# Performance work log

Hardware: AMD Instinct MI355X
Metric: run time of the kernel (lower is better)

## Reference

```python
import jax, jax.numpy as jnp
import numpy as np

BETA = 0.95
THR = 1.0  # snntorch Leaky default threshold

# Heaviside spike with ATan surrogate gradient (snntorch default, alpha=2):
# d/dx = 1 / (1 + (pi*x)^2)
@jax.custom_vjp
def spike_fn(x):
    return (x > 0).astype(x.dtype)

def _spike_fwd(x):
    return spike_fn(x), x

def _spike_bwd(x, g):
    return (g / (1.0 + (jnp.pi * x) ** 2),)

spike_fn.defvjp(_spike_fwd, _spike_bwd)


def setup_inputs() -> dict:
    key = jax.random.key(0)
    ks = jax.random.split(key, 5)
    T, B, D_in, D_h, D_out = 25, 4096, 784, 1000, 10
    x = jax.random.normal(ks[0], (T, B, D_in), dtype=jnp.float32)
    # Kaiming-uniform-ish init like nn.Linear
    w1 = jax.random.uniform(ks[1], (D_h, D_in), jnp.float32, -1, 1) / np.sqrt(D_in)
    b1 = jax.random.uniform(ks[2], (D_h,), jnp.float32, -1, 1) / np.sqrt(D_in)
    w2 = jax.random.uniform(ks[3], (D_out, D_h), jnp.float32, -1, 1) / np.sqrt(D_h)
    b2 = jax.random.uniform(ks[4], (D_out,), jnp.float32, -1, 1) / np.sqrt(D_h)
    return {"x": x, "w1": w1, "b1": b1, "w2": w2, "b2": b2}


def reference(x, w1, b1, w2, b2):
    B = x.shape[1]
    mem1_0 = jnp.zeros((B, w1.shape[0]), x.dtype)
    mem2_0 = jnp.zeros((B, w2.shape[0]), x.dtype)

    def step(carry, xt):
        mem1, mem2 = carry
        # layer 1: Linear + Leaky (reset-by-subtraction, reset from prior mem)
        cur1 = xt @ w1.T + b1
        reset1 = spike_fn(mem1 - THR)
        mem1 = BETA * mem1 + cur1 - reset1 * THR
        spk1 = spike_fn(mem1 - THR)
        # layer 2
        cur2 = spk1 @ w2.T + b2
        reset2 = spike_fn(mem2 - THR)
        mem2 = BETA * mem2 + cur2 - reset2 * THR
        spk2 = spike_fn(mem2 - THR)
        return (mem1, mem2), spk2

    (mem1, mem2), spk_rec = jax.lax.scan(step, (mem1_0, mem2_0), x)
    return spk_rec, mem2
```

## Files before the change

### kernel.cpp

```cpp
#include <hip/hip_runtime.h>

typedef _Float16 f16;
typedef _Float16 f16x4 __attribute__((ext_vector_type(4)));
typedef _Float16 f16x8 __attribute__((ext_vector_type(8)));
typedef float f32x4 __attribute__((ext_vector_type(4)));

#define T_STEPS 25
#define BATCH   4096
#define DIN     784
#define DH      1000
#define HP      1024
#define DOUT    10
#define MROWS   (T_STEPS * BATCH)
#define KSEG    800
#define KA      (2 * KSEG)
#define KB      (3 * KSEG)
#define NTILES  (KB / 32)

__global__ void aconv_kernel(const float* __restrict__ x, f16* __restrict__ Ah)
{
    const int total = MROWS * 200;
    for (int idx = blockIdx.x * blockDim.x + threadIdx.x; idx < total;
         idx += gridDim.x * blockDim.x) {
        const int r  = idx / 200;
        const int c4 = (idx - r * 200) * 4;
        f16x4 hi, lo;
        if (c4 < DIN) {
            const float4 v = *(const float4*)(x + (size_t)r * DIN + c4);
            const float vv[4] = {v.x, v.y, v.z, v.w};
            #pragma unroll
            for (int j = 0; j < 4; ++j) {
                f16 h = (f16)vv[j];
                hi[j] = h;
                lo[j] = (f16)(vv[j] - (float)h);
            }
        } else {
            #pragma unroll
            for (int j = 0; j < 4; ++j) { hi[j] = (f16)0.f; lo[j] = (f16)0.f; }
        }
        *(f16x4*)(Ah + (size_t)r * KA + c4)        = hi;
        *(f16x4*)(Ah + (size_t)r * KA + KSEG + c4) = lo;
    }
}

__global__ void wconv_kernel(const float* __restrict__ w1, const float* __restrict__ b1,
                             const float* __restrict__ w2,
                             f16* __restrict__ Wh, float* __restrict__ b1p,
                             float* __restrict__ w2t)
{
    const int stride = gridDim.x * blockDim.x;
    const int tid0 = blockIdx.x * blockDim.x + threadIdx.x;
    for (int idx = tid0; idx < HP * KB; idx += stride) {
        const int n  = idx / KB;
        const int k  = idx - n * KB;
        const int seg = k / KSEG;
        const int kc  = k - seg * KSEG;
        float w = (n < DH && kc < DIN) ? w1[n * DIN + kc] : 0.f;
        f16 h = (f16)w;
        Wh[idx] = (seg < 2) ? h : (f16)(w - (float)h);
    }
    for (int idx = tid0; idx < HP; idx += stride)
        b1p[idx] = (idx < DH) ? b1[idx] : 0.f;
    for (int idx = tid0; idx < HP * DOUT; idx += stride) {
        const int h = idx / DOUT;
        const int o = idx - h * DOUT;
        w2t[idx] = (h < DH) ? w2[o * DH + h] : 0.f;
    }
}

#define GL(gp, ldsoff) __builtin_amdgcn_global_load_lds( \
    (const __attribute__((address_space(1))) void*)(gp), \
    (__attribute__((address_space(3))) void*)(lds + (ldsoff)), 16, 0, 0)

#define STAGE_A(tt) do { \
    const int ak_ = (((tt) < 50) ? (tt) : ((tt) - 50)) * 32; \
    GL(Ag + ak_,            ((tt) & 3) * 8192 + widoff); \
    GL(Ag + ak_ + 128 * KA, ((tt) & 3) * 8192 + 4096 + widoff); } while (0)
#define STAGE_B(tt) do { \
    const int bk_ = (tt) * 32; \
    GL(Bg + bk_,                     32768 + ((tt) & 3) * 8192 + widoff); \
    GL(Bg + bk_ + (size_t)128 * KB,  32768 + ((tt) & 3) * 8192 + 4096 + widoff); } while (0)

#define MFMA16(A0, A1, A2, A3, B0, B1, B2, B3, M0) \
    acc[M0+0][0] = __builtin_amdgcn_mfma_f32_16x16x32_f16(A0, B0, acc[M0+0][0], 0, 0, 0); \
    acc[M0+0][1] = __builtin_amdgcn_mfma_f32_16x16x32_f16(A0, B1, acc[M0+0][1], 0, 0, 0); \
    acc[M0+0][2] = __builtin_amdgcn_mfma_f32_16x16x32_f16(A0, B2, acc[M0+0][2], 0, 0, 0); \
    acc[M0+0][3] = __builtin_amdgcn_mfma_f32_16x16x32_f16(A0, B3, acc[M0+0][3], 0, 0, 0); \
    acc[M0+1][0] = __builtin_amdgcn_mfma_f32_16x16x32_f16(A1, B0, acc[M0+1][0], 0, 0, 0); \
    acc[M0+1][1] = __builtin_amdgcn_mfma_f32_16x16x32_f16(A1, B1, acc[M0+1][1], 0, 0, 0); \
    acc[M0+1][2] = __builtin_amdgcn_mfma_f32_16x16x32_f16(A1, B2, acc[M0+1][2], 0, 0, 0); \
    acc[M0+1][3] = __builtin_amdgcn_mfma_f32_16x16x32_f16(A1, B3, acc[M0+1][3], 0, 0, 0); \
    acc[M0+2][0] = __builtin_amdgcn_mfma_f32_16x16x32_f16(A2, B0, acc[M0+2][0], 0, 0, 0); \
    acc[M0+2][1] = __builtin_amdgcn_mfma_f32_16x16x32_f16(A2, B1, acc[M0+2][1], 0, 0, 0); \
    acc[M0+2][2] = __builtin_amdgcn_mfma_f32_16x16x32_f16(A2, B2, acc[M0+2][2], 0, 0, 0); \
    acc[M0+2][3] = __builtin_amdgcn_mfma_f32_16x16x32_f16(A2, B3, acc[M0+2][3], 0, 0, 0); \
    acc[M0+3][0] = __builtin_amdgcn_mfma_f32_16x16x32_f16(A3, B0, acc[M0+3][0], 0, 0, 0); \
    acc[M0+3][1] = __builtin_amdgcn_mfma_f32_16x16x32_f16(A3, B1, acc[M0+3][1], 0, 0, 0); \
    acc[M0+3][2] = __builtin_amdgcn_mfma_f32_16x16x32_f16(A3, B2, acc[M0+3][2], 0, 0, 0); \
    acc[M0+3][3] = __builtin_amdgcn_mfma_f32_16x16x32_f16(A3, B3, acc[M0+3][3], 0, 0, 0);

#define BODY(tt, aI0,aI1,aI2,aI3, bI0,bI1,bI2,bI3, aO0,aO1,aO2,aO3, bO0,bO1,bO2,bO3, STG, VMWSTR) do { \
    const int bcur = ((tt) & 3) * 8192; \
    const int bnxt = (((tt) + 1) & 3) * 8192; \
    if (STG) { STAGE_A((tt) + 3); STAGE_B((tt) + 3); } \
    asm volatile("s_waitcnt lgkmcnt(0)" ::: "memory");    \
    __builtin_amdgcn_sched_barrier(0); \
    ah0 = *(const f16x8*)(lds + bcur + aoffb + 4 * 512); \
    ah1 = *(const f16x8*)(lds + bcur + aoffb + 5 * 512); \
    ah2 = *(const f16x8*)(lds + bcur + aoffb + 6 * 512); \
    ah3 = *(const f16x8*)(lds + bcur + aoffb + 7 * 512); \
    __builtin_amdgcn_sched_barrier(0); \
    __builtin_amdgcn_s_setprio(1); \
    MFMA16(aI0, aI1, aI2, aI3, bI0, bI1, bI2, bI3, 0)     \
    __builtin_amdgcn_s_setprio(0); \
    asm volatile("s_waitcnt lgkmcnt(0)" ::: "memory");    \
    __builtin_amdgcn_sched_barrier(0); \
    asm volatile(VMWSTR ::: "memory"); \
    __builtin_amdgcn_s_barrier();                         \
    aO0 = *(const f16x8*)(lds + bnxt + aoffb + 0 * 512); \
    aO1 = *(const f16x8*)(lds + bnxt + aoffb + 1 * 512); \
    aO2 = *(const f16x8*)(lds + bnxt + aoffb + 2 * 512); \
    aO3 = *(const f16x8*)(lds + bnxt + aoffb + 3 * 512); \
    bO0 = *(const f16x8*)(lds + 32768 + bnxt + boffb + 0 * 512); \
    bO1 = *(const f16x8*)(lds + 32768 + bnxt + boffb + 1 * 512); \
    bO2 = *(const f16x8*)(lds + 32768 + bnxt + boffb + 2 * 512); \
    bO3 = *(const f16x8*)(lds + 32768 + bnxt + boffb + 3 * 512); \
    __builtin_amdgcn_sched_barrier(0); \
    __builtin_amdgcn_s_setprio(1); \
    MFMA16(ah0, ah1, ah2, ah3, bI0, bI1, bI2, bI3, 4)     \
    __builtin_amdgcn_s_setprio(0); \
} while (0)

#define BODY_(...) BODY(__VA_ARGS__)

#define SET_A aA0,aA1,aA2,aA3, bA0,bA1,bA2,bA3
#define SET_B aB0,aB1,aB2,aB3, bB0,bB1,bB2,bB3

__global__ __launch_bounds__(512, 2)
void gemm_kernel(const f16* __restrict__ A, const f16* __restrict__ B,
                 const float* __restrict__ bias, float* __restrict__ C)
{
    __shared__ f16 lds[65536];

    const int bid = blockIdx.x;
    const int swz = (bid & 7) * 200 + (bid >> 3);
    const int mt = swz >> 2;
    const int nt = swz & 3;
    const size_t rowBase = (size_t)mt * 256;
    const int colBase = nt * 256;

    const int tid  = threadIdx.x;
    const int wid  = tid >> 6;
    const int lane = tid & 63;
    const int wm = wid >> 2;
    const int wn = wid & 3;

    const int srow = tid >> 2;
    const int g = (tid & 3) ^ ((tid >> 3) & 3);
    const f16* Ag = A + (rowBase + srow) * KA + g * 8;
    const f16* Bg = B + (size_t)(colBase + srow) * KB + g * 8;
    const int widoff = wid * 512;

    const int cq = (lane >> 4) ^ (((lane & 15) >> 1) & 3);
    const int aoffb = (wm * 128 + (lane & 15)) * 32 + cq * 8;
    const int boffb = (wn * 64  + (lane & 15)) * 32 + cq * 8;

    f32x4 acc[8][4];
    #pragma unroll
    for (int m = 0; m < 8; ++m)
        #pragma unroll
        for (int n = 0; n < 4; ++n)
            acc[m][n] = (f32x4){0.f, 0.f, 0.f, 0.f};

    f16x8 aA0, aA1, aA2, aA3, bA0, bA1, bA2, bA3;
    f16x8 aB0, aB1, aB2, aB3, bB0, bB1, bB2, bB3;
    f16x8 ah0, ah1, ah2, ah3;

    STAGE_A(0); STAGE_B(0);
    STAGE_A(1); STAGE_B(1);
    STAGE_A(2); STAGE_B(2);
    asm volatile("s_waitcnt vmcnt(8)" ::: "memory");
    __builtin_amdgcn_s_barrier();
    aA0 = *(const f16x8*)(lds + aoffb + 0 * 512);
    aA1 = *(const f16x8*)(lds + aoffb + 1 * 512);
    aA2 = *(const f16x8*)(lds + aoffb + 2 * 512);
    aA3 = *(const f16x8*)(lds + aoffb + 3 * 512);
    bA0 = *(const f16x8*)(lds + 32768 + boffb + 0 * 512);
    bA1 = *(const f16x8*)(lds + 32768 + boffb + 1 * 512);
    bA2 = *(const f16x8*)(lds + 32768 + boffb + 2 * 512);
    bA3 = *(const f16x8*)(lds + 32768 + boffb + 3 * 512);

    for (int t = 0; t < NTILES - 3; t += 2) {
        BODY_(t,     SET_A, SET_B, 1, "s_waitcnt vmcnt(8)");
        BODY_(t + 1, SET_B, SET_A, 1, "s_waitcnt vmcnt(8)");
    }
    BODY_(NTILES - 3, SET_A, SET_B, 0, "s_waitcnt vmcnt(4)");
    BODY_(NTILES - 2, SET_B, SET_A, 0, "s_waitcnt vmcnt(0)");
    {
        const int bcur = ((NTILES - 1) & 3) * 8192;
        asm volatile("s_waitcnt lgkmcnt(0)" ::: "memory");
        __builtin_amdgcn_sched_barrier(0);
        ah0 = *(const f16x8*)(lds + bcur + aoffb + 4 * 512);
        ah1 = *(const f16x8*)(lds + bcur + aoffb + 5 * 512);
        ah2 = *(const f16x8*)(lds + bcur + aoffb + 6 * 512);
        ah3 = *(const f16x8*)(lds + bcur + aoffb + 7 * 512);
        __builtin_amdgcn_sched_barrier(0);
        MFMA16(aA0, aA1, aA2, aA3, bA0, bA1, bA2, bA3, 0)
        asm volatile("s_waitcnt lgkmcnt(0)" ::: "memory");
        __builtin_amdgcn_sched_barrier(0);
        MFMA16(ah0, ah1, ah2, ah3, bA0, bA1, bA2, bA3, 4)
    }

    const int c_col0 = colBase + wn * 64 + (lane & 15);
    const size_t c_row0 = rowBase + wm * 128 + (lane >> 4) * 4;
    #pragma unroll
    for (int n = 0; n < 4; ++n) {
        const int gcol = c_col0 + n * 16;
        const float bv = bias[gcol];
        #pragma unroll
        for (int m = 0; m < 8; ++m) {
            const size_t grow = c_row0 + m * 16;
            #pragma unroll
            for (int r = 0; r < 4; ++r)
                C[(grow + r) * HP + gcol] = acc[m][n][r] + bv;
        }
    }
}

__global__ __launch_bounds__(256)
void phase2_kernel(const float* __restrict__ cur1, const float* __restrict__ w2t,
                   const float* __restrict__ b2, float* __restrict__ out)
{
    __shared__ float w2s[HP * DOUT];
    const int tid = threadIdx.x;
    for (int i = tid; i < HP * DOUT; i += 256) w2s[i] = w2t[i];

    const int lane = tid & 63;
    const int wave = tid >> 6;
    const int b = blockIdx.x * 4 + wave;

    float m1[16];
    #pragma unroll
    for (int i = 0; i < 16; ++i) m1[i] = 0.f;
    float m2[DOUT], b2r[DOUT];
    #pragma unroll
    for (int o = 0; o < DOUT; ++o) { m2[o] = 0.f; b2r[o] = b2[o]; }
    __syncthreads();

    for (int t = 0; t < T_STEPS; ++t) {
        const float* cr = cur1 + ((size_t)t * BATCH + b) * HP;
        float p[DOUT];
        #pragma unroll
        for (int o = 0; o < DOUT; ++o) p[o] = 0.f;

        #pragma unroll
        for (int c = 0; c < 4; ++c) {
            const float4 cu = *(const float4*)(cr + c * 256 + lane * 4);
            const float cv[4] = {cu.x, cu.y, cu.z, cu.w};
            #pragma unroll
            for (int j = 0; j < 4; ++j) {
                const float mo = m1[c * 4 + j];
                const float rs = (mo > 1.0f) ? 1.0f : 0.0f;
                const float mn = 0.95f * mo + cv[j] - rs;
                m1[c * 4 + j] = mn;
                if (mn > 1.0f) {
                    const float* wr = w2s + (c * 256 + lane * 4 + j) * DOUT;
                    #pragma unroll
                    for (int o = 0; o < DOUT; ++o) p[o] += wr[o];
                }
            }
        }
        #pragma unroll
        for (int o = 0; o < DOUT; ++o) {
            float v = p[o];
            #pragma unroll
            for (int msk = 32; msk > 0; msk >>= 1) v += __shfl_xor(v, msk, 64);
            p[o] = v;
        }
        #pragma unroll
        for (int o = 0; o < DOUT; ++o) {
            const float cur2 = p[o] + b2r[o];
            const float mo = m2[o];
            const float rs = (mo > 1.0f) ? 1.0f : 0.0f;
            m2[o] = 0.95f * mo + cur2 - rs;
        }
        if (lane < DOUT)
            out[(size_t)t * (BATCH * DOUT) + (size_t)b * DOUT + lane] =
                (m2[lane] > 1.0f) ? 1.0f : 0.0f;
    }
    if (lane < DOUT)
        out[(size_t)T_STEPS * BATCH * DOUT + (size_t)b * DOUT + lane] = m2[lane];
}

extern "C" void kernel_launch(void* const* d_in, const int* in_sizes, int n_in,
                              void* d_out, int out_size, void* d_ws, size_t ws_size,
                              hipStream_t stream)
{
    const float* x  = (const float*)d_in[0];
    const float* w1 = (const float*)d_in[1];
    const float* b1 = (const float*)d_in[2];
    const float* w2 = (const float*)d_in[3];
    const float* b2 = (const float*)d_in[4];
    float* out = (float*)d_out;

    char* wsb = (char*)d_ws;
    f16*   Ah   = (f16*)(wsb);
    f16*   Wh   = (f16*)(wsb + 327680000);
    float* cur1 = (float*)(wsb + 327680000 + 4915200);
    float* b1p  = (float*)(wsb + 327680000 + 4915200 + 419430400);
    float* w2t  = (float*)(wsb + 327680000 + 4915200 + 419430400 + 4096);

    aconv_kernel<<<4096, 256, 0, stream>>>(x, Ah);
    wconv_kernel<<<1024, 256, 0, stream>>>(w1, b1, w2, Wh, b1p, w2t);
    gemm_kernel<<<1600, 512, 0, stream>>>(Ah, Wh, b1p, cur1);
    phase2_kernel<<<1024, 256, 0, stream>>>(cur1, w2t, b2, out);
}
```

Baseline: 772.0 us.

## Switch GEMM to 64-wide K tiles with double-buffered LDS staging

The main GEMM now stages 64-wide K tiles into two LDS buffers instead of 32-wide tiles in a four-deep ring, with an 8-wide XOR swizzle for the new row pitch. The weight matrix is padded to 2432 columns so the K loop divides evenly into 38 tiles, and the workspace offsets are adjusted to match. The aim is to halve the number of barrier and wait points per unit of K and to give each wave more MFMA work between synchronisations. In exchange, prefetch runs only one tile ahead, with a full vmcnt(0) wait each iteration, so global-load latency may be less well hidden.

```diff
diff --git a/kernel.cpp b/kernel.cpp
--- a/kernel.cpp
+++ b/kernel.cpp
@@ -15,7 +15,8 @@
 #define KSEG    800
 #define KA      (2 * KSEG)
 #define KB      (3 * KSEG)
-#define NTILES  (KB / 32)
+#define WROW    2432
+#define NT64    38
 
 __global__ void aconv_kernel(const float* __restrict__ x, f16* __restrict__ Ah)
 {
@@ -50,14 +51,18 @@
 {
     const int stride = gridDim.x * blockDim.x;
     const int tid0 = blockIdx.x * blockDim.x + threadIdx.x;
-    for (int idx = tid0; idx < HP * KB; idx += stride) {
-        const int n  = idx / KB;
-        const int k  = idx - n * KB;
-        const int seg = k / KSEG;
-        const int kc  = k - seg * KSEG;
-        float w = (n < DH && kc < DIN) ? w1[n * DIN + kc] : 0.f;
-        f16 h = (f16)w;
-        Wh[idx] = (seg < 2) ? h : (f16)(w - (float)h);
+    for (int idx = tid0; idx < HP * WROW; idx += stride) {
+        const int n  = idx / WROW;
+        const int k  = idx - n * WROW;
+        f16 v = (f16)0.f;
+        if (k < KB) {
+            const int seg = k / KSEG;
+            const int kc  = k - seg * KSEG;
+            float w = (n < DH && kc < DIN) ? w1[n * DIN + kc] : 0.f;
+            f16 h = (f16)w;
+            v = (seg < 2) ? h : (f16)(w - (float)h);
+        }
+        Wh[idx] = v;
     }
     for (int idx = tid0; idx < HP; idx += stride)
         b1p[idx] = (idx < DH) ? b1[idx] : 0.f;
@@ -72,14 +77,18 @@
     (const __attribute__((address_space(1))) void*)(gp), \
     (__attribute__((address_space(3))) void*)(lds + (ldsoff)), 16, 0, 0)
 
-#define STAGE_A(tt) do { \
-    const int ak_ = (((tt) < 50) ? (tt) : ((tt) - 50)) * 32; \
-    GL(Ag + ak_,            ((tt) & 3) * 8192 + widoff); \
-    GL(Ag + ak_ + 128 * KA, ((tt) & 3) * 8192 + 4096 + widoff); } while (0)
-#define STAGE_B(tt) do { \
-    const int bk_ = (tt) * 32; \
-    GL(Bg + bk_,                     32768 + ((tt) & 3) * 8192 + widoff); \
-    GL(Bg + bk_ + (size_t)128 * KB,  32768 + ((tt) & 3) * 8192 + 4096 + widoff); } while (0)
+#define STAGE64(tt) do { \
+    const int _buf = ((tt) & 1) * 16384; \
+    const int _ak  = (((tt) < 25) ? (tt) : ((tt) - 25)) * 64; \
+    const int _bk  = (tt) * 64; \
+    GL(Ag + _ak + 0 * 64 * KA,   _buf + 0 * 4096 + widoff); \
+    GL(Ag + _ak + 1 * 64 * KA,   _buf + 1 * 4096 + widoff); \
+    GL(Ag + _ak + 2 * 64 * KA,   _buf + 2 * 4096 + widoff); \
+    GL(Ag + _ak + 3 * 64 * KA,   _buf + 3 * 4096 + widoff); \
+    GL(Bg + _bk + 0 * 64 * WROW, 32768 + _buf + 0 * 4096 + widoff); \
+    GL(Bg + _bk + 1 * 64 * WROW, 32768 + _buf + 1 * 4096 + widoff); \
+    GL(Bg + _bk + 2 * 64 * WROW, 32768 + _buf + 2 * 4096 + widoff); \
+    GL(Bg + _bk + 3 * 64 * WROW, 32768 + _buf + 3 * 4096 + widoff); } while (0)
 
 #define MFMA16(A0, A1, A2, A3, B0, B1, B2, B3, M0) \
     acc[M0+0][0] = __builtin_amdgcn_mfma_f32_16x16x32_f16(A0, B0, acc[M0+0][0], 0, 0, 0); \
@@ -99,42 +108,65 @@
     acc[M0+3][2] = __builtin_amdgcn_mfma_f32_16x16x32_f16(A3, B2, acc[M0+3][2], 0, 0, 0); \
     acc[M0+3][3] = __builtin_amdgcn_mfma_f32_16x16x32_f16(A3, B3, acc[M0+3][3], 0, 0, 0);
 
-#define BODY(tt, aI0,aI1,aI2,aI3, bI0,bI1,bI2,bI3, aO0,aO1,aO2,aO3, bO0,bO1,bO2,bO3, STG, VMWSTR) do { \
-    const int bcur = ((tt) & 3) * 8192; \
-    const int bnxt = (((tt) + 1) & 3) * 8192; \
-    if (STG) { STAGE_A((tt) + 3); STAGE_B((tt) + 3); } \
-    asm volatile("s_waitcnt lgkmcnt(0)" ::: "memory");    \
-    __builtin_amdgcn_sched_barrier(0); \
-    ah0 = *(const f16x8*)(lds + bcur + aoffb + 4 * 512); \
-    ah1 = *(const f16x8*)(lds + bcur + aoffb + 5 * 512); \
-    ah2 = *(const f16x8*)(lds + bcur + aoffb + 6 * 512); \
-    ah3 = *(const f16x8*)(lds + bcur + aoffb + 7 * 512); \
+#define RD(off) (*(const f16x8*)(lds + (off)))
+
+#define BODY64(tt, STG) do { \
+    const int bufc = ((tt) & 1) * 16384; \
+    f16x8 b00, b01, b02, b03, a00, a01, a02, a03, a10, a11, a12, a13; \
+    f16x8 b10, b11, b12, b13, c00, c01, c02, c03, c10, c11, c12, c13; \
+    if (STG) STAGE64((tt) + 1); \
+     \
+    b00 = RD(bbase + bufc + 0 * 1024 + cA0); \
+    b01 = RD(bbase + bufc + 1 * 1024 + cA0); \
+    b02 = RD(bbase + bufc + 2 * 1024 + cA0); \
+    b03 = RD(bbase + bufc + 3 * 1024 + cA0); \
+    a00 = RD(abase + bufc + 0 * 1024 + cA0); \
+    a01 = RD(abase + bufc + 1 * 1024 + cA0); \
+    a02 = RD(abase + bufc + 2 * 1024 + cA0); \
+    a03 = RD(abase + bufc + 3 * 1024 + cA0); \
+    a10 = RD(abase + bufc + 4096 + 0 * 1024 + cA0); \
+    a11 = RD(abase + bufc + 4096 + 1 * 1024 + cA0); \
+    a12 = RD(abase + bufc + 4096 + 2 * 1024 + cA0); \
+    a13 = RD(abase + bufc + 4096 + 3 * 1024 + cA0); \
+    asm volatile("s_waitcnt lgkmcnt(4)" ::: "memory");   \
     __builtin_amdgcn_sched_barrier(0); \
     __builtin_amdgcn_s_setprio(1); \
-    MFMA16(aI0, aI1, aI2, aI3, bI0, bI1, bI2, bI3, 0)     \
+    MFMA16(a00, a01, a02, a03, b00, b01, b02, b03, 0) \
     __builtin_amdgcn_s_setprio(0); \
-    asm volatile("s_waitcnt lgkmcnt(0)" ::: "memory");    \
-    __builtin_amdgcn_sched_barrier(0); \
-    asm volatile(VMWSTR ::: "memory"); \
-    __builtin_amdgcn_s_barrier();                         \
-    aO0 = *(const f16x8*)(lds + bnxt + aoffb + 0 * 512); \
-    aO1 = *(const f16x8*)(lds + bnxt + aoffb + 1 * 512); \
-    aO2 = *(const f16x8*)(lds + bnxt + aoffb + 2 * 512); \
-    aO3 = *(const f16x8*)(lds + bnxt + aoffb + 3 * 512); \
-    bO0 = *(const f16x8*)(lds + 32768 + bnxt + boffb + 0 * 512); \
-    bO1 = *(const f16x8*)(lds + 32768 + bnxt + boffb + 1 * 512); \
-    bO2 = *(const f16x8*)(lds + 32768 + bnxt + boffb + 2 * 512); \
-    bO3 = *(const f16x8*)(lds + 32768 + bnxt + boffb + 3 * 512); \
+    asm volatile("s_waitcnt lgkmcnt(0)" ::: "memory");   \
+    __builtin_amdgcn_sched_barrier(0); \
+     \
+    b10 = RD(bbase + bufc + 0 * 1024 + cA1); \
+    b11 = RD(bbase + bufc + 1 * 1024 + cA1); \
+    b12 = RD(bbase + bufc + 2 * 1024 + cA1); \
+    b13 = RD(bbase + bufc + 3 * 1024 + cA1); \
+    c00 = RD(abase + bufc + 0 * 1024 + cA1); \
+    c01 = RD(abase + bufc + 1 * 1024 + cA1); \
+    c02 = RD(abase + bufc + 2 * 1024 + cA1); \
+    c03 = RD(abase + bufc + 3 * 1024 + cA1); \
+    c10 = RD(abase + bufc + 4096 + 0 * 1024 + cA1); \
+    c11 = RD(abase + bufc + 4096 + 1 * 1024 + cA1); \
+    c12 = RD(abase + bufc + 4096 + 2 * 1024 + cA1); \
+    c13 = RD(abase + bufc + 4096 + 3 * 1024 + cA1); \
     __builtin_amdgcn_sched_barrier(0); \
     __builtin_amdgcn_s_setprio(1); \
-    MFMA16(ah0, ah1, ah2, ah3, bI0, bI1, bI2, bI3, 4)     \
+    MFMA16(a10, a11, a12, a13, b00, b01, b02, b03, 4) \
     __builtin_amdgcn_s_setprio(0); \
+    asm volatile("s_waitcnt lgkmcnt(4)" ::: "memory");   \
+    __builtin_amdgcn_sched_barrier(0); \
+    __builtin_amdgcn_s_setprio(1); \
+    MFMA16(c00, c01, c02, c03, b10, b11, b12, b13, 0) \
+    __builtin_amdgcn_s_setprio(0); \
+    asm volatile("s_waitcnt lgkmcnt(0)" ::: "memory");   \
+    __builtin_amdgcn_sched_barrier(0); \
+    __builtin_amdgcn_s_setprio(1); \
+    MFMA16(c10, c11, c12, c13, b10, b11, b12, b13, 4) \
+    __builtin_amdgcn_s_setprio(0); \
+    if (STG) { \
+        asm volatile("s_waitcnt vmcnt(0)" ::: "memory");   \
+        __builtin_amdgcn_s_barrier(); \
+    } \
 } while (0)
-
-#define BODY_(...) BODY(__VA_ARGS__)
-
-#define SET_A aA0,aA1,aA2,aA3, bA0,bA1,bA2,bA3
-#define SET_B aB0,aB1,aB2,aB3, bB0,bB1,bB2,bB3
 
 __global__ __launch_bounds__(512, 2)
 void gemm_kernel(const f16* __restrict__ A, const f16* __restrict__ B,
@@ -155,15 +187,15 @@
     const int wm = wid >> 2;
     const int wn = wid & 3;
 
-    const int srow = tid >> 2;
-    const int g = (tid & 3) ^ ((tid >> 3) & 3);
-    const f16* Ag = A + (rowBase + srow) * KA + g * 8;
-    const f16* Bg = B + (size_t)(colBase + srow) * KB + g * 8;
+    const int gsw = (tid & 7) ^ ((tid >> 3) & 7);
+    const f16* Ag = A + (rowBase + (tid >> 3)) * KA + gsw * 8;
+    const f16* Bg = B + (size_t)(colBase + (tid >> 3)) * WROW + gsw * 8;
     const int widoff = wid * 512;
 
-    const int cq = (lane >> 4) ^ (((lane & 15) >> 1) & 3);
-    const int aoffb = (wm * 128 + (lane & 15)) * 32 + cq * 8;
-    const int boffb = (wn * 64  + (lane & 15)) * 32 + cq * 8;
+    const int cA0 = (((lane >> 4))     ^ (lane & 7)) * 8;
+    const int cA1 = (((lane >> 4) + 4) ^ (lane & 7)) * 8;
+    const int abase = (wm * 128 + (lane & 15)) * 64;
+    const int bbase = 32768 + (wn * 64 + (lane & 15)) * 64;
 
     f32x4 acc[8][4];
     #pragma unroll
@@ -172,44 +204,16 @@
         for (int n = 0; n < 4; ++n)
             acc[m][n] = (f32x4){0.f, 0.f, 0.f, 0.f};
 
-    f16x8 aA0, aA1, aA2, aA3, bA0, bA1, bA2, bA3;
-    f16x8 aB0, aB1, aB2, aB3, bB0, bB1, bB2, bB3;
-    f16x8 ah0, ah1, ah2, ah3;
-
-    STAGE_A(0); STAGE_B(0);
-    STAGE_A(1); STAGE_B(1);
-    STAGE_A(2); STAGE_B(2);
-    asm volatile("s_waitcnt vmcnt(8)" ::: "memory");
+    STAGE64(0);
+    asm volatile("s_waitcnt vmcnt(0)" ::: "memory");
     __builtin_amdgcn_s_barrier();
-    aA0 = *(const f16x8*)(lds + aoffb + 0 * 512);
-    aA1 = *(const f16x8*)(lds + aoffb + 1 * 512);
-    aA2 = *(const f16x8*)(lds + aoffb + 2 * 512);
-    aA3 = *(const f16x8*)(lds + aoffb + 3 * 512);
-    bA0 = *(const f16x8*)(lds + 32768 + boffb + 0 * 512);
-    bA1 = *(const f16x8*)(lds + 32768 + boffb + 1 * 512);
-    bA2 = *(const f16x8*)(lds + 32768 + boffb + 2 * 512);
-    bA3 = *(const f16x8*)(lds + 32768 + boffb + 3 * 512);
-
-    for (int t = 0; t < NTILES - 3; t += 2) {
-        BODY_(t,     SET_A, SET_B, 1, "s_waitcnt vmcnt(8)");
-        BODY_(t + 1, SET_B, SET_A, 1, "s_waitcnt vmcnt(8)");
-    }
-    BODY_(NTILES - 3, SET_A, SET_B, 0, "s_waitcnt vmcnt(4)");
-    BODY_(NTILES - 2, SET_B, SET_A, 0, "s_waitcnt vmcnt(0)");
-    {
-        const int bcur = ((NTILES - 1) & 3) * 8192;
-        asm volatile("s_waitcnt lgkmcnt(0)" ::: "memory");
-        __builtin_amdgcn_sched_barrier(0);
-        ah0 = *(const f16x8*)(lds + bcur + aoffb + 4 * 512);
-        ah1 = *(const f16x8*)(lds + bcur + aoffb + 5 * 512);
-        ah2 = *(const f16x8*)(lds + bcur + aoffb + 6 * 512);
-        ah3 = *(const f16x8*)(lds + bcur + aoffb + 7 * 512);
-        __builtin_amdgcn_sched_barrier(0);
-        MFMA16(aA0, aA1, aA2, aA3, bA0, bA1, bA2, bA3, 0)
-        asm volatile("s_waitcnt lgkmcnt(0)" ::: "memory");
-        __builtin_amdgcn_sched_barrier(0);
-        MFMA16(ah0, ah1, ah2, ah3, bA0, bA1, bA2, bA3, 4)
-    }
+
+    for (int t = 0; t < 36; t += 2) {
+        BODY64(t, 1);
+        BODY64(t + 1, 1);
+    }
+    BODY64(36, 1);
+    BODY64(37, 0);
 
     const int c_col0 = colBase + wn * 64 + (lane & 15);
     const size_t c_row0 = rowBase + wm * 128 + (lane >> 4) * 4;
@@ -306,9 +310,9 @@
     char* wsb = (char*)d_ws;
     f16*   Ah   = (f16*)(wsb);
     f16*   Wh   = (f16*)(wsb + 327680000);
-    float* cur1 = (float*)(wsb + 327680000 + 4915200);
-    float* b1p  = (float*)(wsb + 327680000 + 4915200 + 419430400);
-    float* w2t  = (float*)(wsb + 327680000 + 4915200 + 419430400 + 4096);
+    float* cur1 = (float*)(wsb + 327680000 + 4980736);
+    float* b1p  = (float*)(wsb + 327680000 + 4980736 + 419430400);
+    float* w2t  = (float*)(wsb + 327680000 + 4980736 + 419430400 + 4096);
 
     aconv_kernel<<<4096, 256, 0, stream>>>(x, Ah);
     wconv_kernel<<<1024, 256, 0, stream>>>(w1, b1, w2, Wh, b1p, w2t);
```

After: 746.7 us. 3.3% less time.
